# Kernel optimization log

Hardware: AMD Instinct MI355X
Metric: run time of the kernel (lower is better)

The kernel has to match this reference:

```python
import jax, jax.numpy as jnp
import numpy as np

N_NODES = 100000
N_EDGES = 1600000
IN_DIM = 128
HIDDEN = 128
OUT_DIM = 64


def setup_inputs() -> dict:
    key = jax.random.key(0)
    k_x, k_e, k_w1, k_b1, k_w2, k_b2 = jax.random.split(key, 6)
    x = jax.random.normal(k_x, (N_NODES, IN_DIM), dtype=jnp.float32)
    edge_index = jax.random.randint(k_e, (2, N_EDGES), 0, N_NODES, dtype=jnp.int64)
    # GCNConv weight/bias (glorot-ish scale) and final Linear head
    W1 = jax.random.normal(k_w1, (IN_DIM, HIDDEN), dtype=jnp.float32) / np.sqrt(IN_DIM)
    b1 = jnp.zeros((HIDDEN,), dtype=jnp.float32)
    W2 = jax.random.normal(k_w2, (HIDDEN, OUT_DIM), dtype=jnp.float32) / np.sqrt(HIDDEN)
    b2 = jnp.zeros((OUT_DIM,), dtype=jnp.float32)
    return {"x": x, "W1": W1, "b1": b1, "W2": W2, "b2": b2, "edge_index": edge_index}


def _gcn_conv(x, W, b, src, dst, norm, n_nodes):
    # PyG GCNConv: linear transform, then sym-normalized neighbor aggregation
    h = x @ W                                   # (N, H) dense transform
    msg = h[src] * norm[:, None]                # (E+N, H) gather + scale
    out = jax.ops.segment_sum(msg, dst, num_segments=n_nodes)  # scatter-add
    return out + b


def reference(x, W1, b1, W2, b2, edge_index):
    n = x.shape[0]
    # add self-loops (PyG GCNConv default)
    loop = jnp.arange(n, dtype=edge_index.dtype)
    src = jnp.concatenate([edge_index[0], loop])
    dst = jnp.concatenate([edge_index[1], loop])
    # symmetric normalization D^{-1/2} A D^{-1/2}
    deg = jnp.zeros((n,), dtype=x.dtype).at[dst].add(1.0)
    dinv = jnp.where(deg > 0, jax.lax.rsqrt(jnp.maximum(deg, 1.0)), 0.0)
    norm = dinv[src] * dinv[dst]

    h = _gcn_conv(x, W1, b1, src, dst, norm, n)
    h = jax.nn.relu(h)
    # dropout: identity in eval/inference mode
    return h @ W2 + b2
```

## Files before the change

kernel.cpp:

```cpp
#include <hip/hip_runtime.h>

#define N_NODES 100000
#define N_EDGES 1600000
#define IN_DIM  128
#define HIDDEN  128
#define OUT_DIM 64

#define BUCK_SHIFT 6
#define BUCK_SZ    64
#define NB_BUCK ((N_NODES + BUCK_SZ - 1) / BUCK_SZ)
#define EPB 4096
#define NBLK_E ((N_EDGES + EPB - 1) / EPB)
#define GB1 ((N_NODES + 127) / 128)
#define CAP 1536
#define PCAP 1984

typedef __attribute__((ext_vector_type(8))) short bf8_t;
typedef __attribute__((ext_vector_type(4))) float f4_t;

__device__ __forceinline__ ushort f2b(float f) {
    unsigned int u = __float_as_uint(f);
    u += 0x7fffu + ((u >> 16) & 1u);
    return (ushort)(u >> 16);
}
__device__ __forceinline__ float b2f_lo(unsigned int u) { return __uint_as_float(u << 16); }
__device__ __forceinline__ float b2f_hi(unsigned int u) { return __uint_as_float(u & 0xffff0000u); }

__global__ __launch_bounds__(256) void k_prep(const float* __restrict__ W1,
                                              ushort* __restrict__ w1b,
                                              int* __restrict__ cursor,
                                              float* __restrict__ dinv,
                                              ushort* __restrict__ h) {
    int b = blockIdx.x, t = threadIdx.x;
    if (b < 8) {
        int start = b * 2048;
        #pragma unroll
        for (int j = 0; j < 8; j++) {
            int i = start + j * 256 + t;
            int n = i >> 7, k = i & 127;
            w1b[i] = f2b(W1[k * 128 + n]);
        }
    } else {
        for (int i = t; i < NB_BUCK; i += 256) cursor[i] = 0;
        if (t == 0) dinv[N_NODES] = 0.f;
        if (t < 128) h[(size_t)N_NODES * 128 + t] = 0;
    }
}

__global__ __launch_bounds__(256, 4) void k_fuse1(const int* __restrict__ ei,
                                                  int* __restrict__ cursor,
                                                  unsigned int* __restrict__ part,
                                                  const float* __restrict__ x,
                                                  const ushort* __restrict__ w1b,
                                                  ushort* __restrict__ h) {
    __shared__ __align__(16) ushort smem[128 * 136];
    int tid = threadIdx.x;

    if (blockIdx.x < NBLK_E) {
        int* lh    = (int*)smem;
        int* lbase = lh + NB_BUCK;
        for (int i = tid; i < NB_BUCK; i += 256) lh[i] = 0;
        __syncthreads();
        int e0 = blockIdx.x * EPB;
        int srcv[EPB / 256], dstv[EPB / 256];
        #pragma unroll
        for (int j = 0; j < EPB / 256; j++) {
            int e = e0 + j * 256 + tid;
            if (e < N_EDGES) {
                srcv[j] = ei[e];
                dstv[j] = ei[N_EDGES + e];
                atomicAdd(&lh[dstv[j] >> BUCK_SHIFT], 1);
            } else dstv[j] = -1;
        }
        __syncthreads();
        for (int i = tid; i < NB_BUCK; i += 256) {
            int c = lh[i];
            lbase[i] = (c > 0) ? (i * CAP + atomicAdd(&cursor[i], c)) : 0;
            lh[i] = 0;
        }
        __syncthreads();
        #pragma unroll
        for (int j = 0; j < EPB / 256; j++) {
            if (dstv[j] >= 0) {
                int bk = dstv[j] >> BUCK_SHIFT;
                int pos = lbase[bk] + atomicAdd(&lh[bk], 1);
                part[pos] = ((unsigned int)(dstv[j] & (BUCK_SZ - 1)) << 24) | (unsigned int)srcv[j];
            }
        }
        return;
    }

    typedef ushort (*tile_t)[136];
    tile_t As = (tile_t)smem;
    int row0 = (blockIdx.x - NBLK_E) * 128;
    const int M = N_NODES;

    #pragma unroll
    for (int i = 0; i < 16; i++) {
        int li = tid + i * 256;
        int r = li >> 5, c4 = li & 31;
        int grow = row0 + r; if (grow > M - 1) grow = M - 1;
        float4 v = *(const float4*)(x + (size_t)grow * 128 + c4 * 4);
        ushort4 o;
        o.x = f2b(v.x); o.y = f2b(v.y); o.z = f2b(v.z); o.w = f2b(v.w);
        *(ushort4*)&As[r][c4 * 4] = o;
    }
    __syncthreads();

    int wave = tid >> 6, lane = tid & 63;
    int lr = lane & 15, lq = lane >> 4;
    int wm0 = (wave & 1) * 64;
    int wn0 = (wave >> 1) * 64;

    f4_t acc[4][4];
    #pragma unroll
    for (int mi = 0; mi < 4; mi++)
        #pragma unroll
        for (int ni = 0; ni < 4; ni++) acc[mi][ni] = (f4_t){0.f, 0.f, 0.f, 0.f};

    #pragma unroll
    for (int kb = 0; kb < 4; kb++) {
        bf8_t af[4], bfr[4];
        #pragma unroll
        for (int mi = 0; mi < 4; mi++)
            af[mi] = *(const bf8_t*)&As[wm0 + mi * 16 + lr][kb * 32 + lq * 8];
        #pragma unroll
        for (int ni = 0; ni < 4; ni++)
            bfr[ni] = *(const bf8_t*)(w1b + (size_t)(wn0 + ni * 16 + lr) * 128 + kb * 32 + lq * 8);
        #pragma unroll
        for (int mi = 0; mi < 4; mi++)
            #pragma unroll
            for (int ni = 0; ni < 4; ni++)
                acc[mi][ni] = __builtin_amdgcn_mfma_f32_16x16x32_bf16(
                    af[mi], bfr[ni], acc[mi][ni], 0, 0, 0);
    }

    #pragma unroll
    for (int mi = 0; mi < 4; mi++) {
        #pragma unroll
        for (int r = 0; r < 4; r++) {
            int row = row0 + wm0 + mi * 16 + lq * 4 + r;
            if (row < M) {
                #pragma unroll
                for (int ni = 0; ni < 4; ni++)
                    h[(size_t)row * 128 + wn0 + ni * 16 + lr] = f2b(acc[mi][ni][r]);
            }
        }
    }
}

__global__ __launch_bounds__(256) void k_csr(const unsigned int* __restrict__ part,
                                             const int* __restrict__ cursor,
                                             int* __restrict__ offs,
                                             int* __restrict__ pcnt,
                                             float* __restrict__ dinv,
                                             int* __restrict__ ssrc) {
    __shared__ int ldeg[BUCK_SZ], lsc[BUCK_SZ], lcur[BUCK_SZ], sob[BUCK_SZ];
    __shared__ unsigned int stage[CAP];
    __shared__ int sorted[PCAP];
    int t = threadIdx.x;
    int b = blockIdx.x;
    int rbeg = b * CAP;
    int cnt = cursor[b];
    int node0 = b << BUCK_SHIFT;
    if (t < BUCK_SZ) ldeg[t] = 0;
    for (int i = t; i < PCAP; i += 256) sorted[i] = N_NODES;
    __syncthreads();
    for (int i = t; i < cnt; i += 256) {
        unsigned int u = part[rbeg + i];
        stage[i] = u;
        atomicAdd(&ldeg[u >> 24], 1);
    }
    __syncthreads();
    int v = 0, pv = 0;
    if (t < BUCK_SZ) {
        v = ldeg[t];
        pv = (v + 7) & ~7;
        lsc[t] = pv;
    }
    __syncthreads();
    for (int off = 1; off < BUCK_SZ; off <<= 1) {
        int add = 0;
        if (t < BUCK_SZ && t >= off) add = lsc[t - off];
        __syncthreads();
        if (t < BUCK_SZ) lsc[t] += add;
        __syncthreads();
    }
    if (t < BUCK_SZ) {
        int lob = lsc[t] - pv;
        sob[t] = lob;
        lcur[t] = 0;
        if (node0 + t < N_NODES) {
            offs[node0 + t] = b * PCAP + lob;
            pcnt[node0 + t] = pv;
            dinv[node0 + t] = rsqrtf((float)(v + 1));
        }
    }
    __syncthreads();
    for (int i = t; i < cnt; i += 256) {
        unsigned int u = stage[i];
        int d = u >> 24;
        int pos = atomicAdd(&lcur[d], 1);
        sorted[sob[d] + pos] = (int)(u & 0xFFFFFFu);
    }
    __syncthreads();
    int total = lsc[BUCK_SZ - 1];
    int4* dst4 = (int4*)(ssrc + (size_t)b * PCAP);
    const int4* src4 = (const int4*)sorted;
    for (int i = t; i < (total >> 2); i += 256) dst4[i] = src4[i];
}

__global__ __launch_bounds__(256, 7) void k_agg2(const ushort* __restrict__ h,
                                                 const int* __restrict__ offs,
                                                 const int* __restrict__ pcnt,
                                                 const int* __restrict__ ssrc,
                                                 const float* __restrict__ dinv,
                                                 const float* __restrict__ b1,
                                                 const float* __restrict__ W2,
                                                 const float* __restrict__ b2,
                                                 float* __restrict__ out) {
    __shared__ ushort As[16][136];
    __shared__ ushort Bs[64][136];
    int tid = threadIdx.x;
    int wave = tid >> 6, lane = tid & 63;
    int base = blockIdx.x * 16;

    #pragma unroll
    for (int i = 0; i < 8; i++) {
        int li = tid + i * 256;
        int k = li >> 4, n4 = li & 15;
        float4 v = *(const float4*)(W2 + (size_t)k * 64 + n4 * 4);
        Bs[n4 * 4 + 0][k] = f2b(v.x);
        Bs[n4 * 4 + 1][k] = f2b(v.y);
        Bs[n4 * 4 + 2][k] = f2b(v.z);
        Bs[n4 * 4 + 3][k] = f2b(v.w);
    }

    const unsigned int* hp = (const unsigned int*)h;
    float2 bb = ((const float2*)b1)[lane];

    #pragma unroll 1
    for (int j = 0; j < 4; j++) {
        int r = wave * 4 + j;
        int n = base + r;
        int e0 = __builtin_amdgcn_readfirstlane(offs[n]);
        int iters = __builtin_amdgcn_readfirstlane(pcnt[n]) >> 3;
        const uint4* ip = (const uint4*)(ssrc + e0);

        float ax0 = 0.f, ay0 = 0.f, ax1 = 0.f, ay1 = 0.f;
        float ax2 = 0.f, ay2 = 0.f, ax3 = 0.f, ay3 = 0.f;
        uint4 i0, i1;
        if (iters > 0) { i0 = ip[0]; i1 = ip[1]; }
        for (int it = 0; it < iters; it++) {
            uint4 nx0 = i0, nx1 = i1;
            if (it + 1 < iters) { nx0 = ip[(it + 1) * 2]; nx1 = ip[(it + 1) * 2 + 1]; }
            int s0 = __builtin_amdgcn_readfirstlane((int)i0.x);
            int s1 = __builtin_amdgcn_readfirstlane((int)i0.y);
            int s2 = __builtin_amdgcn_readfirstlane((int)i0.z);
            int s3 = __builtin_amdgcn_readfirstlane((int)i0.w);
            int s4 = __builtin_amdgcn_readfirstlane((int)i1.x);
            int s5 = __builtin_amdgcn_readfirstlane((int)i1.y);
            int s6 = __builtin_amdgcn_readfirstlane((int)i1.z);
            int s7 = __builtin_amdgcn_readfirstlane((int)i1.w);
            unsigned int u0 = (hp + ((unsigned)s0 << 6))[lane];
            unsigned int u1 = (hp + ((unsigned)s1 << 6))[lane];
            unsigned int u2 = (hp + ((unsigned)s2 << 6))[lane];
            unsigned int u3 = (hp + ((unsigned)s3 << 6))[lane];
            unsigned int u4 = (hp + ((unsigned)s4 << 6))[lane];
            unsigned int u5 = (hp + ((unsigned)s5 << 6))[lane];
            unsigned int u6 = (hp + ((unsigned)s6 << 6))[lane];
            unsigned int u7 = (hp + ((unsigned)s7 << 6))[lane];
            float w0 = dinv[s0], w1 = dinv[s1], w2 = dinv[s2], w3 = dinv[s3];
            float w4 = dinv[s4], w5 = dinv[s5], w6 = dinv[s6], w7 = dinv[s7];
            ax0 = fmaf(b2f_lo(u0), w0, ax0); ay0 = fmaf(b2f_hi(u0), w0, ay0);
            ax1 = fmaf(b2f_lo(u1), w1, ax1); ay1 = fmaf(b2f_hi(u1), w1, ay1);
            ax2 = fmaf(b2f_lo(u2), w2, ax2); ay2 = fmaf(b2f_hi(u2), w2, ay2);
            ax3 = fmaf(b2f_lo(u3), w3, ax3); ay3 = fmaf(b2f_hi(u3), w3, ay3);
            ax0 = fmaf(b2f_lo(u4), w4, ax0); ay0 = fmaf(b2f_hi(u4), w4, ay0);
            ax1 = fmaf(b2f_lo(u5), w5, ax1); ay1 = fmaf(b2f_hi(u5), w5, ay1);
            ax2 = fmaf(b2f_lo(u6), w6, ax2); ay2 = fmaf(b2f_hi(u6), w6, ay2);
            ax3 = fmaf(b2f_lo(u7), w7, ax3); ay3 = fmaf(b2f_hi(u7), w7, ay3);
            i0 = nx0; i1 = nx1;
        }
        unsigned int us = hp[(size_t)n * 64 + lane];
        float dn = dinv[n];
        float rx = (ax0 + ax1 + ax2 + ax3 + b2f_lo(us) * dn) * dn + bb.x;
        float ry = (ay0 + ay1 + ay2 + ay3 + b2f_hi(us) * dn) * dn + bb.y;
        rx = rx > 0.f ? rx : 0.f;
        ry = ry > 0.f ? ry : 0.f;
        *(unsigned int*)&As[r][lane * 2] =
            ((unsigned int)f2b(ry) << 16) | (unsigned int)f2b(rx);
    }
    __syncthreads();

    int lr = lane & 15, lq = lane >> 4;
    f4_t acc = (f4_t){0.f, 0.f, 0.f, 0.f};
    #pragma unroll
    for (int kb = 0; kb < 4; kb++) {
        bf8_t af = *(const bf8_t*)&As[lr][kb * 32 + lq * 8];
        bf8_t bf = *(const bf8_t*)&Bs[wave * 16 + lr][kb * 32 + lq * 8];
        acc = __builtin_amdgcn_mfma_f32_16x16x32_bf16(af, bf, acc, 0, 0, 0);
    }
    int col = wave * 16 + lr;
    float bv = b2[col];
    #pragma unroll
    for (int r = 0; r < 4; r++) {
        int node = base + lq * 4 + r;
        out[(size_t)node * 64 + col] = acc[r] + bv;
    }
}


extern "C" void kernel_launch(void* const* d_in, const int* in_sizes, int n_in,
                              void* d_out, int out_size, void* d_ws, size_t ws_size,
                              hipStream_t stream) {
    const float* x  = (const float*)d_in[0];
    const float* W1 = (const float*)d_in[1];
    const float* b1 = (const float*)d_in[2];
    const float* W2 = (const float*)d_in[3];
    const float* b2 = (const float*)d_in[4];
    const int*   ei = (const int*)d_in[5];
    float* out = (float*)d_out;

    char* w = (char*)d_ws;
    size_t off = 0;
    auto alloc = [&](size_t bytes) -> void* {
        void* p = w + off;
        off += (bytes + 255) & ~(size_t)255;
        return p;
    };
    ushort* h      = (ushort*)alloc((size_t)(N_NODES + 1) * HIDDEN * 2);
    float* dinv    = (float*)alloc((size_t)(N_NODES + 1) * 4);
    int*   offs    = (int*)alloc((size_t)N_NODES * 4);
    int*   pcnt    = (int*)alloc((size_t)N_NODES * 4);
    int*   ssrc    = (int*)alloc((size_t)NB_BUCK * PCAP * 4);
    unsigned int* part = (unsigned int*)alloc((size_t)NB_BUCK * CAP * 4);
    int*   cursor  = (int*)alloc((size_t)NB_BUCK * 4);
    ushort* w1b    = (ushort*)alloc((size_t)HIDDEN * IN_DIM * 2);

    k_prep<<<9, 256, 0, stream>>>(W1, w1b, cursor, dinv, h);
    k_fuse1<<<NBLK_E + GB1, 256, 0, stream>>>(ei, cursor, part, x, w1b, h);
    k_csr<<<NB_BUCK, 256, 0, stream>>>(part, cursor, offs, pcnt, dinv, ssrc);
    k_agg2<<<N_NODES / 16, 256, 0, stream>>>(h, offs, pcnt, ssrc, dinv, b1, W2, b2, out);
}
```

Measured before the change: 204.3 us.

## Fuse CSR bucket sort into aggregation kernel, sorting neighbors in LDS

Merges the per-bucket CSR build into the aggregation kernel, so each block sorts its 64-node bucket's edges in shared memory and aggregates directly from LDS. This removes the global ssrc/offs/pcnt round trip. A lightweight degree kernel still computes dinv first, because aggregation needs every source node's dinv. W2 is pre-converted to bf16 once in the prep kernel and read from global, so blocks no longer transpose it into LDS. Blocks now handle 64 nodes instead of 16, giving fewer, larger blocks with more LDS, and the part array is read twice.

```diff
diff --git a/kernel.cpp b/kernel.cpp
--- a/kernel.cpp
+++ b/kernel.cpp
@@ -27,7 +27,9 @@
 __device__ __forceinline__ float b2f_hi(unsigned int u) { return __uint_as_float(u & 0xffff0000u); }
 
 __global__ __launch_bounds__(256) void k_prep(const float* __restrict__ W1,
+                                              const float* __restrict__ W2,
                                               ushort* __restrict__ w1b,
+                                              ushort* __restrict__ w2b,
                                               int* __restrict__ cursor,
                                               float* __restrict__ dinv,
                                               ushort* __restrict__ h) {
@@ -39,6 +41,14 @@
             int i = start + j * 256 + t;
             int n = i >> 7, k = i & 127;
             w1b[i] = f2b(W1[k * 128 + n]);
+        }
+    } else if (b < 12) {
+        int start = (b - 8) * 2048;
+        #pragma unroll
+        for (int j = 0; j < 8; j++) {
+            int i = start + j * 256 + t;
+            int n = i >> 7, k = i & 127;
+            w2b[i] = f2b(W2[k * 64 + n]);
         }
     } else {
         for (int i = t; i < NB_BUCK; i += 256) cursor[i] = 0;
@@ -149,28 +159,43 @@
     }
 }
 
-__global__ __launch_bounds__(256) void k_csr(const unsigned int* __restrict__ part,
+__global__ __launch_bounds__(256) void k_deg(const unsigned int* __restrict__ part,
                                              const int* __restrict__ cursor,
-                                             int* __restrict__ offs,
-                                             int* __restrict__ pcnt,
-                                             float* __restrict__ dinv,
-                                             int* __restrict__ ssrc) {
-    __shared__ int ldeg[BUCK_SZ], lsc[BUCK_SZ], lcur[BUCK_SZ], sob[BUCK_SZ];
-    __shared__ unsigned int stage[CAP];
-    __shared__ int sorted[PCAP];
-    int t = threadIdx.x;
-    int b = blockIdx.x;
-    int rbeg = b * CAP;
+                                             float* __restrict__ dinv) {
+    __shared__ int ldeg[BUCK_SZ];
+    int t = threadIdx.x, b = blockIdx.x;
     int cnt = cursor[b];
     int node0 = b << BUCK_SHIFT;
     if (t < BUCK_SZ) ldeg[t] = 0;
+    __syncthreads();
+    for (int i = t; i < cnt; i += 256)
+        atomicAdd(&ldeg[part[(size_t)b * CAP + i] >> 24], 1);
+    __syncthreads();
+    if (t < BUCK_SZ && node0 + t < N_NODES)
+        dinv[node0 + t] = rsqrtf((float)(ldeg[t] + 1));
+}
+
+__global__ __launch_bounds__(256, 6) void k_agg3(const ushort* __restrict__ h,
+                                                 const unsigned int* __restrict__ part,
+                                                 const int* __restrict__ cursor,
+                                                 const float* __restrict__ dinv,
+                                                 const float* __restrict__ b1,
+                                                 const ushort* __restrict__ w2b,
+                                                 const float* __restrict__ b2,
+                                                 float* __restrict__ out) {
+    __shared__ int ldeg[BUCK_SZ], lsc[BUCK_SZ], lcur[BUCK_SZ], sob[BUCK_SZ];
+    __shared__ int sorted[PCAP];
+    __shared__ ushort As[BUCK_SZ][136];
+    int t = threadIdx.x, b = blockIdx.x;
+    size_t rbeg = (size_t)b * CAP;
+    int cnt = cursor[b];
+    int node0 = b << BUCK_SHIFT;
+
+    if (t < BUCK_SZ) ldeg[t] = 0;
     for (int i = t; i < PCAP; i += 256) sorted[i] = N_NODES;
     __syncthreads();
-    for (int i = t; i < cnt; i += 256) {
-        unsigned int u = part[rbeg + i];
-        stage[i] = u;
-        atomicAdd(&ldeg[u >> 24], 1);
-    }
+    for (int i = t; i < cnt; i += 256)
+        atomicAdd(&ldeg[part[rbeg + i] >> 24], 1);
     __syncthreads();
     int v = 0, pv = 0;
     if (t < BUCK_SZ) {
@@ -187,126 +212,100 @@
         __syncthreads();
     }
     if (t < BUCK_SZ) {
-        int lob = lsc[t] - pv;
-        sob[t] = lob;
+        sob[t] = lsc[t] - pv;
         lcur[t] = 0;
-        if (node0 + t < N_NODES) {
-            offs[node0 + t] = b * PCAP + lob;
-            pcnt[node0 + t] = pv;
-            dinv[node0 + t] = rsqrtf((float)(v + 1));
-        }
     }
     __syncthreads();
     for (int i = t; i < cnt; i += 256) {
-        unsigned int u = stage[i];
+        unsigned int u = part[rbeg + i];
         int d = u >> 24;
         int pos = atomicAdd(&lcur[d], 1);
         sorted[sob[d] + pos] = (int)(u & 0xFFFFFFu);
     }
     __syncthreads();
-    int total = lsc[BUCK_SZ - 1];
-    int4* dst4 = (int4*)(ssrc + (size_t)b * PCAP);
-    const int4* src4 = (const int4*)sorted;
-    for (int i = t; i < (total >> 2); i += 256) dst4[i] = src4[i];
-}
-
-__global__ __launch_bounds__(256, 7) void k_agg2(const ushort* __restrict__ h,
-                                                 const int* __restrict__ offs,
-                                                 const int* __restrict__ pcnt,
-                                                 const int* __restrict__ ssrc,
-                                                 const float* __restrict__ dinv,
-                                                 const float* __restrict__ b1,
-                                                 const float* __restrict__ W2,
-                                                 const float* __restrict__ b2,
-                                                 float* __restrict__ out) {
-    __shared__ ushort As[16][136];
-    __shared__ ushort Bs[64][136];
-    int tid = threadIdx.x;
-    int wave = tid >> 6, lane = tid & 63;
-    int base = blockIdx.x * 16;
-
-    #pragma unroll
-    for (int i = 0; i < 8; i++) {
-        int li = tid + i * 256;
-        int k = li >> 4, n4 = li & 15;
-        float4 v = *(const float4*)(W2 + (size_t)k * 64 + n4 * 4);
-        Bs[n4 * 4 + 0][k] = f2b(v.x);
-        Bs[n4 * 4 + 1][k] = f2b(v.y);
-        Bs[n4 * 4 + 2][k] = f2b(v.z);
-        Bs[n4 * 4 + 3][k] = f2b(v.w);
-    }
-
+
+    int wave = t >> 6, lane = t & 63;
     const unsigned int* hp = (const unsigned int*)h;
     float2 bb = ((const float2*)b1)[lane];
 
     #pragma unroll 1
-    for (int j = 0; j < 4; j++) {
-        int r = wave * 4 + j;
-        int n = base + r;
-        int e0 = __builtin_amdgcn_readfirstlane(offs[n]);
-        int iters = __builtin_amdgcn_readfirstlane(pcnt[n]) >> 3;
-        const uint4* ip = (const uint4*)(ssrc + e0);
-
-        float ax0 = 0.f, ay0 = 0.f, ax1 = 0.f, ay1 = 0.f;
-        float ax2 = 0.f, ay2 = 0.f, ax3 = 0.f, ay3 = 0.f;
-        uint4 i0, i1;
-        if (iters > 0) { i0 = ip[0]; i1 = ip[1]; }
-        for (int it = 0; it < iters; it++) {
-            uint4 nx0 = i0, nx1 = i1;
-            if (it + 1 < iters) { nx0 = ip[(it + 1) * 2]; nx1 = ip[(it + 1) * 2 + 1]; }
-            int s0 = __builtin_amdgcn_readfirstlane((int)i0.x);
-            int s1 = __builtin_amdgcn_readfirstlane((int)i0.y);
-            int s2 = __builtin_amdgcn_readfirstlane((int)i0.z);
-            int s3 = __builtin_amdgcn_readfirstlane((int)i0.w);
-            int s4 = __builtin_amdgcn_readfirstlane((int)i1.x);
-            int s5 = __builtin_amdgcn_readfirstlane((int)i1.y);
-            int s6 = __builtin_amdgcn_readfirstlane((int)i1.z);
-            int s7 = __builtin_amdgcn_readfirstlane((int)i1.w);
-            unsigned int u0 = (hp + ((unsigned)s0 << 6))[lane];
-            unsigned int u1 = (hp + ((unsigned)s1 << 6))[lane];
-            unsigned int u2 = (hp + ((unsigned)s2 << 6))[lane];
-            unsigned int u3 = (hp + ((unsigned)s3 << 6))[lane];
-            unsigned int u4 = (hp + ((unsigned)s4 << 6))[lane];
-            unsigned int u5 = (hp + ((unsigned)s5 << 6))[lane];
-            unsigned int u6 = (hp + ((unsigned)s6 << 6))[lane];
-            unsigned int u7 = (hp + ((unsigned)s7 << 6))[lane];
-            float w0 = dinv[s0], w1 = dinv[s1], w2 = dinv[s2], w3 = dinv[s3];
-            float w4 = dinv[s4], w5 = dinv[s5], w6 = dinv[s6], w7 = dinv[s7];
-            ax0 = fmaf(b2f_lo(u0), w0, ax0); ay0 = fmaf(b2f_hi(u0), w0, ay0);
-            ax1 = fmaf(b2f_lo(u1), w1, ax1); ay1 = fmaf(b2f_hi(u1), w1, ay1);
-            ax2 = fmaf(b2f_lo(u2), w2, ax2); ay2 = fmaf(b2f_hi(u2), w2, ay2);
-            ax3 = fmaf(b2f_lo(u3), w3, ax3); ay3 = fmaf(b2f_hi(u3), w3, ay3);
-            ax0 = fmaf(b2f_lo(u4), w4, ax0); ay0 = fmaf(b2f_hi(u4), w4, ay0);
-            ax1 = fmaf(b2f_lo(u5), w5, ax1); ay1 = fmaf(b2f_hi(u5), w5, ay1);
-            ax2 = fmaf(b2f_lo(u6), w6, ax2); ay2 = fmaf(b2f_hi(u6), w6, ay2);
-            ax3 = fmaf(b2f_lo(u7), w7, ax3); ay3 = fmaf(b2f_hi(u7), w7, ay3);
-            i0 = nx0; i1 = nx1;
-        }
-        unsigned int us = hp[(size_t)n * 64 + lane];
-        float dn = dinv[n];
-        float rx = (ax0 + ax1 + ax2 + ax3 + b2f_lo(us) * dn) * dn + bb.x;
-        float ry = (ay0 + ay1 + ay2 + ay3 + b2f_hi(us) * dn) * dn + bb.y;
-        rx = rx > 0.f ? rx : 0.f;
-        ry = ry > 0.f ? ry : 0.f;
-        *(unsigned int*)&As[r][lane * 2] =
-            ((unsigned int)f2b(ry) << 16) | (unsigned int)f2b(rx);
+    for (int j = 0; j < 16; j++) {
+        int ln = wave * 16 + j;
+        int n = node0 + ln;
+        if (n < N_NODES) {
+            int lsob = __builtin_amdgcn_readfirstlane(sob[ln]);
+            int iters = (__builtin_amdgcn_readfirstlane(ldeg[ln]) + 7) >> 3;
+            const int* sp = sorted + lsob;
+
+            float ax0 = 0.f, ay0 = 0.f, ax1 = 0.f, ay1 = 0.f;
+            float ax2 = 0.f, ay2 = 0.f, ax3 = 0.f, ay3 = 0.f;
+            for (int it = 0; it < iters; it++) {
+                int4 q0 = *(const int4*)(sp + it * 8);
+                int4 q1 = *(const int4*)(sp + it * 8 + 4);
+                int s0 = __builtin_amdgcn_readfirstlane(q0.x);
+                int s1 = __builtin_amdgcn_readfirstlane(q0.y);
+                int s2 = __builtin_amdgcn_readfirstlane(q0.z);
+                int s3 = __builtin_amdgcn_readfirstlane(q0.w);
+                int s4 = __builtin_amdgcn_readfirstlane(q1.x);
+                int s5 = __builtin_amdgcn_readfirstlane(q1.y);
+                int s6 = __builtin_amdgcn_readfirstlane(q1.z);
+                int s7 = __builtin_amdgcn_readfirstlane(q1.w);
+                unsigned int u0 = (hp + ((unsigned)s0 << 6))[lane];
+                unsigned int u1 = (hp + ((unsigned)s1 << 6))[lane];
+                unsigned int u2 = (hp + ((unsigned)s2 << 6))[lane];
+                unsigned int u3 = (hp + ((unsigned)s3 << 6))[lane];
+                unsigned int u4 = (hp + ((unsigned)s4 << 6))[lane];
+                unsigned int u5 = (hp + ((unsigned)s5 << 6))[lane];
+                unsigned int u6 = (hp + ((unsigned)s6 << 6))[lane];
+                unsigned int u7 = (hp + ((unsigned)s7 << 6))[lane];
+                float w0 = dinv[s0], w1 = dinv[s1], w2 = dinv[s2], w3 = dinv[s3];
+                float w4 = dinv[s4], w5 = dinv[s5], w6 = dinv[s6], w7 = dinv[s7];
+                ax0 = fmaf(b2f_lo(u0), w0, ax0); ay0 = fmaf(b2f_hi(u0), w0, ay0);
+                ax1 = fmaf(b2f_lo(u1), w1, ax1); ay1 = fmaf(b2f_hi(u1), w1, ay1);
+                ax2 = fmaf(b2f_lo(u2), w2, ax2); ay2 = fmaf(b2f_hi(u2), w2, ay2);
+                ax3 = fmaf(b2f_lo(u3), w3, ax3); ay3 = fmaf(b2f_hi(u3), w3, ay3);
+                ax0 = fmaf(b2f_lo(u4), w4, ax0); ay0 = fmaf(b2f_hi(u4), w4, ay0);
+                ax1 = fmaf(b2f_lo(u5), w5, ax1); ay1 = fmaf(b2f_hi(u5), w5, ay1);
+                ax2 = fmaf(b2f_lo(u6), w6, ax2); ay2 = fmaf(b2f_hi(u6), w6, ay2);
+                ax3 = fmaf(b2f_lo(u7), w7, ax3); ay3 = fmaf(b2f_hi(u7), w7, ay3);
+            }
+            unsigned int us = hp[(size_t)n * 64 + lane];
+            float dn = rsqrtf((float)(__builtin_amdgcn_readfirstlane(ldeg[ln]) + 1));
+            float rx = (ax0 + ax1 + ax2 + ax3 + b2f_lo(us) * dn) * dn + bb.x;
+            float ry = (ay0 + ay1 + ay2 + ay3 + b2f_hi(us) * dn) * dn + bb.y;
+            rx = rx > 0.f ? rx : 0.f;
+            ry = ry > 0.f ? ry : 0.f;
+            *(unsigned int*)&As[ln][lane * 2] =
+                ((unsigned int)f2b(ry) << 16) | (unsigned int)f2b(rx);
+        } else {
+            *(unsigned int*)&As[ln][lane * 2] = 0;
+        }
     }
     __syncthreads();
 
     int lr = lane & 15, lq = lane >> 4;
-    f4_t acc = (f4_t){0.f, 0.f, 0.f, 0.f};
+    f4_t acc[4];
+    #pragma unroll
+    for (int mi = 0; mi < 4; mi++) acc[mi] = (f4_t){0.f, 0.f, 0.f, 0.f};
     #pragma unroll
     for (int kb = 0; kb < 4; kb++) {
-        bf8_t af = *(const bf8_t*)&As[lr][kb * 32 + lq * 8];
-        bf8_t bf = *(const bf8_t*)&Bs[wave * 16 + lr][kb * 32 + lq * 8];
-        acc = __builtin_amdgcn_mfma_f32_16x16x32_bf16(af, bf, acc, 0, 0, 0);
+        bf8_t bfv = *(const bf8_t*)(w2b + (size_t)(wave * 16 + lr) * 128 + kb * 32 + lq * 8);
+        #pragma unroll
+        for (int mi = 0; mi < 4; mi++) {
+            bf8_t af = *(const bf8_t*)&As[mi * 16 + lr][kb * 32 + lq * 8];
+            acc[mi] = __builtin_amdgcn_mfma_f32_16x16x32_bf16(af, bfv, acc[mi], 0, 0, 0);
+        }
     }
     int col = wave * 16 + lr;
     float bv = b2[col];
     #pragma unroll
-    for (int r = 0; r < 4; r++) {
-        int node = base + lq * 4 + r;
-        out[(size_t)node * 64 + col] = acc[r] + bv;
+    for (int mi = 0; mi < 4; mi++) {
+        #pragma unroll
+        for (int r = 0; r < 4; r++) {
+            int node = node0 + mi * 16 + lq * 4 + r;
+            if (node < N_NODES)
+                out[(size_t)node * 64 + col] = acc[mi][r] + bv;
+        }
     }
 }
 
@@ -331,15 +330,13 @@
     };
     ushort* h      = (ushort*)alloc((size_t)(N_NODES + 1) * HIDDEN * 2);
     float* dinv    = (float*)alloc((size_t)(N_NODES + 1) * 4);
-    int*   offs    = (int*)alloc((size_t)N_NODES * 4);
-    int*   pcnt    = (int*)alloc((size_t)N_NODES * 4);
-    int*   ssrc    = (int*)alloc((size_t)NB_BUCK * PCAP * 4);
     unsigned int* part = (unsigned int*)alloc((size_t)NB_BUCK * CAP * 4);
     int*   cursor  = (int*)alloc((size_t)NB_BUCK * 4);
     ushort* w1b    = (ushort*)alloc((size_t)HIDDEN * IN_DIM * 2);
-
-    k_prep<<<9, 256, 0, stream>>>(W1, w1b, cursor, dinv, h);
+    ushort* w2b    = (ushort*)alloc((size_t)OUT_DIM * HIDDEN * 2);
+
+    k_prep<<<13, 256, 0, stream>>>(W1, W2, w1b, w2b, cursor, dinv, h);
     k_fuse1<<<NBLK_E + GB1, 256, 0, stream>>>(ei, cursor, part, x, w1b, h);
-    k_csr<<<NB_BUCK, 256, 0, stream>>>(part, cursor, offs, pcnt, dinv, ssrc);
-    k_agg2<<<N_NODES / 16, 256, 0, stream>>>(h, offs, pcnt, ssrc, dinv, b1, W2, b2, out);
-}
+    k_deg<<<NB_BUCK, 256, 0, stream>>>(part, cursor, dinv);
+    k_agg3<<<NB_BUCK, 256, 0, stream>>>(h, part, cursor, dinv, b1, w2b, b2, out);
+}
```

Result: slower. 218.8 us (+7.1%).
